# Performance work log

Measured on AMD Instinct MI355X. Metric: run time of the kernel, lower is better.

Reference implementation:

```python
import jax, jax.numpy as jnp
import numpy as np

L = 4        # n_layers_time
D = 128      # d_model
H = 8        # n_heads
T = 12       # n_time_bins (= max_n_time_bins)
E = 128      # n_electrodes
B = 2        # batch
S = 2        # n_samples (1 positive + 1 negative)
OUT = 1      # dim_output
ROPE_SCALE = 10000.0
HD = D // H          # head_dim = 16
HD4 = HD // 4        # rotated half-pair width = 4
EPS = 1e-5


def _rope_tables():
    # theta = scale ** ((-arange(0, hd//2, 2) / hd) // 2)  -- faithful to torch precedence
    a = jnp.arange(0, HD // 2, 2, dtype=jnp.float32)
    theta = ROPE_SCALE ** jnp.floor((-a / HD) / 2.0)       # [HD4]
    pe = jnp.arange(T, dtype=jnp.float32)[:, None] * theta  # [T, HD4]
    pe = pe.reshape(1, 1, T, 1, 1, HD4)
    return jnp.sin(pe), jnp.cos(pe)


def _causal_mask():
    return jnp.triu(jnp.ones((T, T), dtype=bool), k=1)  # True = masked


def layer_norm(x, g, b):
    m = jnp.mean(x, axis=-1, keepdims=True)
    v = jnp.mean(jnp.square(x - m), axis=-1, keepdims=True)
    return (x - m) * jax.lax.rsqrt(v + EPS) * g + b


def apply_rope(x, sin, cos):
    # x: [B, S, T, E, H, HD]
    xl = x[..., :HD4]
    xr = x[..., HD4:2 * HD4]
    xu = x[..., 2 * HD4:]
    return jnp.concatenate([xl * cos + xr * sin, xr * cos - xl * sin, xu], axis=-1)


def attention(q_in, k_in, v_in, Wq, bq, Wk, bk, Wv, bv, Wo, bo, sin, cos, causal):
    Bq, Sq, Tq, Eq, Dm = q_in.shape
    Sk = k_in.shape[1]
    proj = lambda x, W, b, Ss: (x @ W.T + b).reshape(Bq, Ss, Tq, Eq, H, HD)
    q = apply_rope(proj(q_in, Wq, bq, Sq), sin, cos)
    k = apply_rope(proj(k_in, Wk, bk, Sk), sin, cos)
    v = proj(v_in, Wv, bv, Sk)
    # flatten (S,T,E) -> seq
    qf = q.transpose(0, 4, 1, 2, 3, 5).reshape(Bq, H, Sq * Tq * Eq, HD)
    kf = k.transpose(0, 4, 1, 2, 3, 5).reshape(Bq, H, Sk * Tq * Eq, HD)
    vf = v.transpose(0, 4, 1, 2, 3, 5).reshape(Bq, H, Sk * Tq * Eq, HD)
    scores = jnp.einsum('bhqd,bhkd->bhqk', qf, kf) * (float(HD) ** -0.5)
    scores = scores.reshape(Bq, H, Sq, Tq, Eq, Sk, Tq, Eq)
    mask = causal[None, None, None, :, None, None, :, None]  # causal over time only
    scores = jnp.where(mask, -jnp.inf, scores)
    scores = scores.reshape(Bq, H, Sq * Tq * Eq, Sk * Tq * Eq)
    attnw = jax.nn.softmax(scores, axis=-1)
    attnw = jnp.where(jnp.isnan(attnw), 0.0, attnw)
    out = jnp.einsum('bhqk,bhkd->bhqd', attnw, vf)
    out = out.reshape(Bq, H, Sq, Tq, Eq, HD).transpose(0, 2, 3, 4, 1, 5).reshape(Bq, Sq, Tq, Eq, Dm)
    return out @ Wo.T + bo


def setup_inputs() -> dict:
    key = jax.random.key(0)
    ks = jax.random.split(key, 16)
    w = lambda k, shape: jax.random.normal(k, shape, dtype=jnp.float32) * 0.02
    inp = {
        'x': jax.random.normal(ks[0], (B, S, T, E, D), dtype=jnp.float32),
        'Wq': w(ks[1], (L, D, D)), 'bq': jnp.zeros((L, D), jnp.float32),
        'Wk': w(ks[2], (L, D, D)), 'bk': jnp.zeros((L, D), jnp.float32),
        'Wv': w(ks[3], (L, D, D)), 'bv': jnp.zeros((L, D), jnp.float32),
        'Wo': w(ks[4], (L, D, D)), 'bo': jnp.zeros((L, D), jnp.float32),
        'W1': w(ks[5], (L, 4 * D, D)), 'b1': jnp.zeros((L, 4 * D), jnp.float32),
        'W2': w(ks[6], (L, D, 4 * D)), 'b2': jnp.zeros((L, D), jnp.float32),
        'g1': jnp.ones((L, D), jnp.float32), 'bn1': jnp.zeros((L, D), jnp.float32),
        'g2': jnp.ones((L, D), jnp.float32), 'bn2': jnp.zeros((L, D), jnp.float32),
        'Wf': w(ks[7], (OUT, D)), 'bf': jnp.zeros((OUT,), jnp.float32),
    }
    return inp


def reference(x, Wq, bq, Wk, bk, Wv, bv, Wo, bo, W1, b1, W2, b2, g1, bn1, g2, bn2, Wf, bf):
    sin, cos = _rope_tables()
    causal = _causal_mask()
    for i in range(L):
        x2 = layer_norm(x, g1[i], bn1[i])
        kv = x2[:, :1]
        x_pos = attention(x2[:, :1], kv, kv, Wq[i], bq[i], Wk[i], bk[i], Wv[i], bv[i], Wo[i], bo[i], sin, cos, causal)
        x_neg = attention(x2[:, 1:], kv, kv, Wq[i], bq[i], Wk[i], bk[i], Wv[i], bv[i], Wo[i], bo[i], sin, cos, causal)
        x = jnp.concatenate([x[:, :1] + x_pos, x[:, 1:] + x_neg], axis=1)
        x2 = layer_norm(x, g2[i], bn2[i])
        h = jax.nn.gelu(x2 @ W1[i].T + b1[i], approximate=False)
        x = x + h @ W2[i].T + b2[i]
    return x @ Wf.T + bf
```

## Files before the change

### kernel.cpp

```cpp
#include <hip/hip_runtime.h>
#include <hip/hip_bf16.h>
#include <math.h>

#define LAYERS 4
#define DIM    128
#define NH     8
#define TT     12
#define EE     128
#define BB     2
#define SS     2
#define HD     16
#define DFF    512
#define NROWS  (BB*SS*TT*EE)
#define NKROWS (BB*TT*EE)

typedef __attribute__((ext_vector_type(8)))  short bf16x8;
typedef __attribute__((ext_vector_type(4)))  short short4v;
typedef __attribute__((ext_vector_type(4)))  float f32x4;
typedef __attribute__((ext_vector_type(16))) float f32x16;

#define MFMA32 __builtin_amdgcn_mfma_f32_32x32x16_bf16

__device__ __forceinline__ unsigned short f2bf(float f) {
    union { float f; unsigned u; } x; x.f = f;
    unsigned r = x.u + 0x7fffu + ((x.u >> 16) & 1u);
    return (unsigned short)(r >> 16);
}

__device__ __forceinline__ unsigned cvtpk(float a, float b) {
    unsigned r;
    asm("v_cvt_pk_bf16_f32 %0, %1, %2" : "=v"(r) : "v"(a), "v"(b));
    return r;
}

union U8 { unsigned u[4]; bf16x8 v; };

__global__ __launch_bounds__(256) void wconv_kernel(const float* __restrict__ Wq,
        const float* __restrict__ Wk, const float* __restrict__ Wv,
        const float* __restrict__ Wo, const float* __restrict__ W1,
        const float* __restrict__ W2, short* __restrict__ wbuf) {
    int idx = (blockIdx.x * 256 + threadIdx.x) * 4;
    const float* src; int off;
    if      (idx < 65536)  { src = Wq; off = idx; }
    else if (idx < 131072) { src = Wk; off = idx - 65536; }
    else if (idx < 196608) { src = Wv; off = idx - 131072; }
    else if (idx < 262144) { src = Wo; off = idx - 196608; }
    else if (idx < 524288) { src = W1; off = idx - 262144; }
    else                   { src = W2; off = idx - 524288; }
    float4 v = *(const float4*)(src + off);
    short4v o = { (short)f2bf(v.x), (short)f2bf(v.y), (short)f2bf(v.z), (short)f2bf(v.w) };
    *(short4v*)(wbuf + idx) = o;
}

__global__ __launch_bounds__(256) void ln_kernel(const float* __restrict__ x,
                                                 short* __restrict__ y,
                                                 const float* __restrict__ g,
                                                 const float* __restrict__ b) {
    int wave = threadIdx.x >> 6, lane = threadIdx.x & 63;
    int row = blockIdx.x * 4 + wave;
    const float* xp = x + (size_t)row * DIM;
    float2 v = *(const float2*)(xp + lane * 2);
    float s = v.x + v.y, sq = v.x * v.x + v.y * v.y;
    #pragma unroll
    for (int o = 1; o < 64; o <<= 1) { s += __shfl_xor(s, o); sq += __shfl_xor(sq, o); }
    float mean = s * (1.0f / 128.0f);
    float var = sq * (1.0f / 128.0f) - mean * mean;
    float rs = 1.0f / sqrtf(var + 1e-5f);
    float2 gv = *(const float2*)(g + lane * 2);
    float2 bv = *(const float2*)(b + lane * 2);
    float ox = (v.x - mean) * rs * gv.x + bv.x;
    float oy = (v.y - mean) * rs * gv.y + bv.y;
    unsigned u = (unsigned)f2bf(ox) | ((unsigned)f2bf(oy) << 16);
    *(unsigned*)(&y[(size_t)row * 128 + lane * 2]) = u;
}

__device__ __forceinline__ void gemm_core32(const short* __restrict__ Ab,
                                            const short* __restrict__ Wb,
                                            int K, f32x16 acc[2]) {
    #pragma unroll 8
    for (int k0 = 0; k0 < K; k0 += 16) {
        bf16x8 a0 = *(const bf16x8*)(Ab + k0);
        bf16x8 a1 = *(const bf16x8*)(Ab + (size_t)32 * K + k0);
        bf16x8 b  = *(const bf16x8*)(Wb + k0);
        acc[0] = MFMA32(a0, b, acc[0], 0, 0, 0);
        acc[1] = MFMA32(a1, b, acc[1], 0, 0, 0);
    }
}

__global__ __launch_bounds__(256) void qkv_kernel(const short* __restrict__ x2b,
        const short* __restrict__ wbuf, const float* __restrict__ bq,
        const float* __restrict__ bk, const float* __restrict__ bv, int layer,
        short* __restrict__ qb, short* __restrict__ kb, short* __restrict__ vt) {
    int z = blockIdx.z, by = blockIdx.y, bx = blockIdx.x;
    if (z > 0 && by >= 24) return;
    const short* Wz = wbuf + (z == 0 ? 0 : z == 1 ? 65536 : 131072) + layer * 16384;
    const float* bz = (z == 0 ? bq : z == 1 ? bk : bv) + layer * 128;
    int r0 = by * 128, c0 = bx * 64;
    int gadd = (z > 0) ? (by / 12) * 1536 : 0;
    int tid = threadIdx.x, wv = tid >> 6, l = tid & 63, l31 = l & 31, hi = l >> 5;
    int wr = wv >> 1, wc = wv & 1;
    const short* Ab = x2b + (size_t)(r0 + gadd + wr * 64 + l31) * 128 + hi * 8;
    const short* Wb = Wz + (size_t)(c0 + wc * 32 + l31) * 128 + hi * 8;
    f32x16 acc[2];
    #pragma unroll
    for (int i = 0; i < 16; ++i) { acc[0][i] = 0.f; acc[1][i] = 0.f; }
    gemm_core32(Ab, Wb, 128, acc);
    int c = c0 + wc * 32 + l31;
    float bb = bz[c];
    int t = by % 12;
    if (z < 2) {
        short* dst = z ? kb : qb;
        float sc = z ? 1.0f : 0.25f;
        int cc = c & 15, i4 = c & 3;
        float theta = (i4 == 0) ? 1.0f : 1e-4f;
        float ang = (float)t * theta;
        float sn = sinf(ang), cs = cosf(ang);
        #pragma unroll
        for (int mi = 0; mi < 2; ++mi)
        #pragma unroll
        for (int reg = 0; reg < 16; ++reg) {
            float v = acc[mi][reg] + bb;
            float pv = __shfl_xor(v, 4);
            float vo = (cc < 4) ? (v * cs + pv * sn)
                     : (cc < 8) ? (v * cs - pv * sn) : v;
            vo *= sc;
            int r = r0 + wr * 64 + mi * 32 + (reg & 3) + 8 * (reg >> 2) + 4 * hi;
            dst[(size_t)r * 128 + c] = (short)f2bf(vo);
        }
    } else {
        int d = c & 15, hh = c >> 4, bidx = by / 12;
        #pragma unroll
        for (int mi = 0; mi < 2; ++mi)
        #pragma unroll
        for (int rq = 0; rq < 4; ++rq) {
            int rcb = r0 + wr * 64 + mi * 32 + 8 * rq + 4 * hi;
            int kk = rcb - bidx * 1536;
            short4v o;
            #pragma unroll
            for (int j = 0; j < 4; ++j) o[j] = (short)f2bf(acc[mi][4 * rq + j] + bb);
            *(short4v*)(vt + ((size_t)(bidx * 8 + hh) * 16 + d) * 1536 + kk) = o;
        }
    }
}

__global__ __launch_bounds__(256) void attn_part(const short* __restrict__ qb,
        const short* __restrict__ kb, const short* __restrict__ vt,
        float* __restrict__ part) {
    int bid = blockIdx.x;
    int blk = bid / 3, sp = bid - blk * 3;
    int tq = 11 - (blk >> 5);
    int hb = blk & 31, h = hb >> 2, bs = hb & 3, b = bs >> 1;
    int tid = threadIdx.x;
    int wv = tid >> 6, l = tid & 63, l31 = l & 31, hi = l >> 5;
    int q0 = (bs * 12 + tq) * 128 + wv * 32;
    bf16x8 qf = *(const bf16x8*)(qb + (size_t)(q0 + l31) * 128 + h * 16 + hi * 8);
    const short* kp = kb + (size_t)(b * 1536 + l31) * 128 + h * 16 + hi * 8;
    const short* vp = vt + ((size_t)(b * 8 + h) * 16 + l31) * 1536 + hi * 8;
    bool vload = l31 < 16;
    f32x16 acc, zv;
    #pragma unroll
    for (int i = 0; i < 16; ++i) { acc[i] = 0.f; zv[i] = 0.f; }
    float m = -1e30f, lsum = 0.f;
    int nch = (tq + 1) * 4;
    for (int c = sp; c < nch; c += 3) {
        bf16x8 kf = *(const bf16x8*)(kp + (size_t)c * 32 * 128);
        f32x16 s = MFMA32(kf, qf, zv, 0, 0, 0);
        float cm = s[0];
        #pragma unroll
        for (int j = 1; j < 16; ++j) cm = fmaxf(cm, s[j]);
        cm = fmaxf(cm, __shfl_xor(cm, 32));
        float mn = fmaxf(m, cm);
        float corr = __expf(m - mn);
        m = mn;
        float p[16]; float ps = 0.f;
        #pragma unroll
        for (int j = 0; j < 16; ++j) { p[j] = __expf(s[j] - mn); ps += p[j]; }
        ps += __shfl_xor(ps, 32);
        lsum = lsum * corr + ps;
        #pragma unroll
        for (int r = 0; r < 8; ++r) acc[r] *= corr;
        unsigned w0 = cvtpk(p[0],  p[1]),  w1 = cvtpk(p[2],  p[3]);
        unsigned w2 = cvtpk(p[4],  p[5]),  w3 = cvtpk(p[6],  p[7]);
        unsigned w4 = cvtpk(p[8],  p[9]),  w5 = cvtpk(p[10], p[11]);
        unsigned w6 = cvtpk(p[12], p[13]), w7 = cvtpk(p[14], p[15]);
        unsigned t1 = hi ? w0 : w2, t2 = hi ? w1 : w3;
        unsigned t3 = hi ? w4 : w6, t4 = hi ? w5 : w7;
        unsigned x1 = __shfl_xor((int)t1, 32), x2 = __shfl_xor((int)t2, 32);
        unsigned x3 = __shfl_xor((int)t3, 32), x4 = __shfl_xor((int)t4, 32);
        U8 pb1, pb2;
        pb1.u[0] = hi ? x1 : w0;  pb1.u[1] = hi ? x2 : w1;
        pb1.u[2] = hi ? w2 : x1;  pb1.u[3] = hi ? w3 : x2;
        pb2.u[0] = hi ? x3 : w4;  pb2.u[1] = hi ? x4 : w5;
        pb2.u[2] = hi ? w6 : x3;  pb2.u[3] = hi ? w7 : x4;
        bf16x8 vf1, vf2;
        #pragma unroll
        for (int i = 0; i < 8; ++i) { vf1[i] = 0; vf2[i] = 0; }
        if (vload) {
            vf1 = *(const bf16x8*)(vp + c * 32);
            vf2 = *(const bf16x8*)(vp + c * 32 + 16);
        }
        acc = MFMA32(vf1, pb1.v, acc, 0, 0, 0);
        acc = MFMA32(vf2, pb2.v, acc, 0, 0, 0);
    }
    float* pp = part + ((size_t)bid * 256 + tid) * 10;
    pp[0] = m; pp[1] = lsum;
    #pragma unroll
    for (int j = 0; j < 8; ++j) pp[2 + j] = acc[j];
}

__global__ __launch_bounds__(256) void attn_comb(const float* __restrict__ part,
        short* __restrict__ attb) {
    int blk = blockIdx.x;
    int tq = 11 - (blk >> 5);
    int hb = blk & 31, h = hb >> 2, bs = hb & 3;
    int tid = threadIdx.x;
    int wv = tid >> 6, l = tid & 63, l31 = l & 31, hi = l >> 5;
    int q0 = (bs * 12 + tq) * 128 + wv * 32;
    const float* p0 = part + ((size_t)(blk * 3) * 256 + tid) * 10;
    const float* p1 = p0 + 2560;
    const float* p2 = p1 + 2560;
    float m0 = p0[0], m1 = p1[0], m2 = p2[0];
    float mm = fmaxf(fmaxf(m0, m1), m2);
    float e0 = __expf(m0 - mm), e1 = __expf(m1 - mm), e2 = __expf(m2 - mm);
    float lsum = p0[1] * e0 + p1[1] * e1 + p2[1] * e2;
    float linv = 1.0f / lsum;
    short4v o1, o2;
    #pragma unroll
    for (int j = 0; j < 4; ++j)
        o1[j] = (short)f2bf((p0[2 + j] * e0 + p1[2 + j] * e1 + p2[2 + j] * e2) * linv);
    #pragma unroll
    for (int j = 0; j < 4; ++j)
        o2[j] = (short)f2bf((p0[6 + j] * e0 + p1[6 + j] * e1 + p2[6 + j] * e2) * linv);
    size_t base = (size_t)(q0 + l31) * 128 + h * 16;
    *(short4v*)(attb + base + 4 * hi) = o1;
    *(short4v*)(attb + base + 8 + 4 * hi) = o2;
}

__global__ __launch_bounds__(256) void res_gemm(const short* __restrict__ A,
        const short* __restrict__ W, const float* __restrict__ bias,
        float* __restrict__ C, int K) {
    int by = blockIdx.y, bx = blockIdx.x;
    int r0 = by * 128, c0 = bx * 64;
    int tid = threadIdx.x, wv = tid >> 6, l = tid & 63, l31 = l & 31, hi = l >> 5;
    int wr = wv >> 1, wc = wv & 1;
    const short* Ab = A + (size_t)(r0 + wr * 64 + l31) * K + hi * 8;
    const short* Wb = W + (size_t)(c0 + wc * 32 + l31) * K + hi * 8;
    f32x16 acc[2];
    #pragma unroll
    for (int i = 0; i < 16; ++i) { acc[0][i] = 0.f; acc[1][i] = 0.f; }
    gemm_core32(Ab, Wb, K, acc);
    int c = c0 + wc * 32 + l31;
    float bb = bias[c];
    #pragma unroll
    for (int mi = 0; mi < 2; ++mi)
    #pragma unroll
    for (int reg = 0; reg < 16; ++reg) {
        int r = r0 + wr * 64 + mi * 32 + (reg & 3) + 8 * (reg >> 2) + 4 * hi;
        C[(size_t)r * 128 + c] += acc[mi][reg] + bb;
    }
}

__global__ __launch_bounds__(256) void gelu_gemm(const short* __restrict__ A,
        const short* __restrict__ W, const float* __restrict__ bias,
        short* __restrict__ H) {
    int by = blockIdx.y, bx = blockIdx.x;
    int r0 = by * 128, c0 = bx * 64;
    int tid = threadIdx.x, wv = tid >> 6, l = tid & 63, l31 = l & 31, hi = l >> 5;
    int wr = wv >> 1, wc = wv & 1;
    const short* Ab = A + (size_t)(r0 + wr * 64 + l31) * 128 + hi * 8;
    const short* Wb = W + (size_t)(c0 + wc * 32 + l31) * 128 + hi * 8;
    f32x16 acc[2];
    #pragma unroll
    for (int i = 0; i < 16; ++i) { acc[0][i] = 0.f; acc[1][i] = 0.f; }
    gemm_core32(Ab, Wb, 128, acc);
    int c = c0 + wc * 32 + l31;
    float bb = bias[c];
    #pragma unroll
    for (int mi = 0; mi < 2; ++mi)
    #pragma unroll
    for (int reg = 0; reg < 16; ++reg) {
        int r = r0 + wr * 64 + mi * 32 + (reg & 3) + 8 * (reg >> 2) + 4 * hi;
        float v = acc[mi][reg] + bb;
        v = 0.5f * v * (1.0f + erff(v * 0.70710678118654752f));
        H[(size_t)r * 512 + c] = (short)f2bf(v);
    }
}

__global__ __launch_bounds__(256) void final_kernel(const float* __restrict__ x,
        const float* __restrict__ Wf, const float* __restrict__ bf,
        float* __restrict__ out) {
    int wave = threadIdx.x >> 6, lane = threadIdx.x & 63;
    int row = blockIdx.x * 4 + wave;
    float2 xv = *(const float2*)(x + (size_t)row * DIM + lane * 2);
    float2 wv = *(const float2*)(Wf + lane * 2);
    float s = xv.x * wv.x + xv.y * wv.y;
    #pragma unroll
    for (int o = 1; o < 64; o <<= 1) s += __shfl_xor(s, o);
    if (lane == 0) out[row] = s + bf[0];
}

extern "C" void kernel_launch(void* const* d_in, const int* in_sizes, int n_in,
                              void* d_out, int out_size, void* d_ws, size_t ws_size,
                              hipStream_t stream) {
    const float* x   = (const float*)d_in[0];
    const float* Wq  = (const float*)d_in[1];
    const float* bq  = (const float*)d_in[2];
    const float* Wk  = (const float*)d_in[3];
    const float* bk  = (const float*)d_in[4];
    const float* Wv  = (const float*)d_in[5];
    const float* bv  = (const float*)d_in[6];
    const float* Wo  = (const float*)d_in[7];
    const float* bo  = (const float*)d_in[8];
    const float* W1  = (const float*)d_in[9];
    const float* b1  = (const float*)d_in[10];
    const float* W2  = (const float*)d_in[11];
    const float* b2  = (const float*)d_in[12];
    const float* g1  = (const float*)d_in[13];
    const float* bn1 = (const float*)d_in[14];
    const float* g2  = (const float*)d_in[15];
    const float* bn2 = (const float*)d_in[16];
    const float* Wf  = (const float*)d_in[17];
    const float* bf  = (const float*)d_in[18];
    float* out = (float*)d_out;

    char* wsb = (char*)d_ws;
    float* xcur  = (float*)(wsb + 0);
    short* x2b   = (short*)(wsb + 3145728);
    short* qb    = (short*)(wsb + 4718592);
    short* kb    = (short*)(wsb + 6291456);
    short* vt    = (short*)(wsb + 7077888);
    short* attb  = (short*)(wsb + 7864320);
    short* hb    = (short*)(wsb + 9437184);
    short* wbuf  = (short*)(wsb + 15728640);
    float* partb = (float*)(wsb + 17301504);

    hipMemcpyAsync(xcur, x, (size_t)NROWS * DIM * sizeof(float),
                   hipMemcpyDeviceToDevice, stream);
    wconv_kernel<<<768, 256, 0, stream>>>(Wq, Wk, Wv, Wo, W1, W2, wbuf);

    for (int i = 0; i < LAYERS; ++i) {
        const short* wob = wbuf + 196608 + i * 16384;
        const short* w1b = wbuf + 262144 + i * 65536;
        const short* w2b = wbuf + 524288 + i * 65536;

        ln_kernel<<<NROWS / 4, 256, 0, stream>>>(xcur, x2b, g1 + i * DIM, bn1 + i * DIM);
        qkv_kernel<<<dim3(2, 48, 3), 256, 0, stream>>>(x2b, wbuf, bq, bk, bv, i, qb, kb, vt);
        attn_part<<<1152, 256, 0, stream>>>(qb, kb, vt, partb);
        attn_comb<<<384, 256, 0, stream>>>(partb, attb);
        res_gemm<<<dim3(2, 48), 256, 0, stream>>>(attb, wob, bo + i * DIM, xcur, 128);
        ln_kernel<<<NROWS / 4, 256, 0, stream>>>(xcur, x2b, g2 + i * DIM, bn2 + i * DIM);
        gelu_gemm<<<dim3(8, 48), 256, 0, stream>>>(x2b, w1b, b1 + i * DFF, hb);
        res_gemm<<<dim3(2, 48), 256, 0, stream>>>(hb, w2b, b2 + i * DIM, xcur, 512);
    }
    final_kernel<<<NROWS / 4, 256, 0, stream>>>(xcur, Wf, bf, out);
}
```

Baseline: 369.2 us.

## Fuse LayerNorm into QKV and FFN1 GEMMs via LDS staging

Removes the standalone LayerNorm kernels. The QKV and FFN1 GEMMs now normalize their 128-row input tile straight into shared memory as bf16, using 512-thread blocks that cover a full 128-column output tile. The initial device-to-device copy of x is dropped: layer 0 reads the input directly, and res_gemm writes res+acc out-of-place. This cuts two launches per layer and the x2 bf16 round trip through global memory. In exchange, FFN1 recomputes LayerNorm four times per row tile, and QKV uses fewer, larger blocks.

Measured after the change: 366.7 us. About the same (-0.7%).

```diff
diff --git a/kernel.cpp b/kernel.cpp
--- a/kernel.cpp
+++ b/kernel.cpp
@@ -16,10 +16,10 @@
 
 typedef __attribute__((ext_vector_type(8)))  short bf16x8;
 typedef __attribute__((ext_vector_type(4)))  short short4v;
-typedef __attribute__((ext_vector_type(4)))  float f32x4;
 typedef __attribute__((ext_vector_type(16))) float f32x16;
 
 #define MFMA32 __builtin_amdgcn_mfma_f32_32x32x16_bf16
+#define CROW(reg) (((reg) & 3) + 8 * ((reg) >> 2) + 4 * hi)
 
 __device__ __forceinline__ unsigned short f2bf(float f) {
     union { float f; unsigned u; } x; x.f = f;
@@ -52,60 +52,74 @@
     *(short4v*)(wbuf + idx) = o;
 }
 
-__global__ __launch_bounds__(256) void ln_kernel(const float* __restrict__ x,
-                                                 short* __restrict__ y,
-                                                 const float* __restrict__ g,
-                                                 const float* __restrict__ b) {
-    int wave = threadIdx.x >> 6, lane = threadIdx.x & 63;
-    int row = blockIdx.x * 4 + wave;
-    const float* xp = x + (size_t)row * DIM;
-    float2 v = *(const float2*)(xp + lane * 2);
-    float s = v.x + v.y, sq = v.x * v.x + v.y * v.y;
-    #pragma unroll
-    for (int o = 1; o < 64; o <<= 1) { s += __shfl_xor(s, o); sq += __shfl_xor(sq, o); }
+__device__ __forceinline__ void ln_to_lds(short (*At)[136], const float* __restrict__ xrow0,
+                                          const float* __restrict__ gl,
+                                          const float* __restrict__ bl, int tid) {
+    int row = tid >> 2, sub = tid & 3;
+    const float* xp = xrow0 + (size_t)row * 128 + sub * 32;
+    float4 v[8];
+    float s = 0.f, q = 0.f;
+    #pragma unroll
+    for (int i = 0; i < 8; ++i) {
+        v[i] = *(const float4*)(xp + i * 4);
+        s += v[i].x + v[i].y + v[i].z + v[i].w;
+        q += v[i].x * v[i].x + v[i].y * v[i].y + v[i].z * v[i].z + v[i].w * v[i].w;
+    }
+    s += __shfl_xor(s, 1); q += __shfl_xor(q, 1);
+    s += __shfl_xor(s, 2); q += __shfl_xor(q, 2);
     float mean = s * (1.0f / 128.0f);
-    float var = sq * (1.0f / 128.0f) - mean * mean;
-    float rs = 1.0f / sqrtf(var + 1e-5f);
-    float2 gv = *(const float2*)(g + lane * 2);
-    float2 bv = *(const float2*)(b + lane * 2);
-    float ox = (v.x - mean) * rs * gv.x + bv.x;
-    float oy = (v.y - mean) * rs * gv.y + bv.y;
-    unsigned u = (unsigned)f2bf(ox) | ((unsigned)f2bf(oy) << 16);
-    *(unsigned*)(&y[(size_t)row * 128 + lane * 2]) = u;
-}
-
-__device__ __forceinline__ void gemm_core32(const short* __restrict__ Ab,
-                                            const short* __restrict__ Wb,
-                                            int K, f32x16 acc[2]) {
+    float rs = 1.0f / sqrtf(q * (1.0f / 128.0f) - mean * mean + 1e-5f);
+    const float* gp = gl + sub * 32;
+    const float* bp = bl + sub * 32;
+    #pragma unroll
+    for (int i = 0; i < 8; ++i) {
+        float4 g4 = *(const float4*)(gp + i * 4);
+        float4 b4 = *(const float4*)(bp + i * 4);
+        unsigned u0 = cvtpk((v[i].x - mean) * rs * g4.x + b4.x,
+                            (v[i].y - mean) * rs * g4.y + b4.y);
+        unsigned u1 = cvtpk((v[i].z - mean) * rs * g4.z + b4.z,
+                            (v[i].w - mean) * rs * g4.w + b4.w);
+        unsigned long long uu = (unsigned long long)u0 | ((unsigned long long)u1 << 32);
+        *(unsigned long long*)(&At[row][sub * 32 + i * 4]) = uu;
+    }
+}
+
+__global__ __launch_bounds__(512) void qkv_lds(const float* __restrict__ xin,
+        const short* __restrict__ wbuf, const float* __restrict__ bq,
+        const float* __restrict__ bk, const float* __restrict__ bv, int layer,
+        const float* __restrict__ gl, const float* __restrict__ bl,
+        short* __restrict__ qb, short* __restrict__ kb, short* __restrict__ vt) {
+    __shared__ short At[128][136];
+    int bid = blockIdx.x;
+    int z, by;
+    if (bid < 48)      { z = 0; by = bid; }
+    else if (bid < 72) { z = 1; by = bid - 48; }
+    else               { z = 2; by = bid - 72; }
+    const short* Wz = wbuf + (z == 0 ? 0 : z == 1 ? 65536 : 131072) + layer * 16384;
+    const float* bz = (z == 0 ? bq : z == 1 ? bk : bv) + layer * 128;
+    int r0 = by * 128;
+    int gadd = (z > 0) ? (by / 12) * 1536 : 0;
+    int tid = threadIdx.x;
+
+    ln_to_lds(At, xin + (size_t)(r0 + gadd) * 128, gl, bl, tid);
+    __syncthreads();
+
+    int wv = tid >> 6, l = tid & 63, l31 = l & 31, hi = l >> 5;
+    int wr = wv >> 2, wc = wv & 3;
+    const short* Wb = Wz + (size_t)(wc * 32 + l31) * 128 + hi * 8;
+    f32x16 acc[2];
+    #pragma unroll
+    for (int i = 0; i < 16; ++i) { acc[0][i] = 0.f; acc[1][i] = 0.f; }
     #pragma unroll 8
-    for (int k0 = 0; k0 < K; k0 += 16) {
-        bf16x8 a0 = *(const bf16x8*)(Ab + k0);
-        bf16x8 a1 = *(const bf16x8*)(Ab + (size_t)32 * K + k0);
+    for (int k0 = 0; k0 < 128; k0 += 16) {
+        bf16x8 a0 = *(const bf16x8*)(&At[wr * 64 + l31][k0 + hi * 8]);
+        bf16x8 a1 = *(const bf16x8*)(&At[wr * 64 + 32 + l31][k0 + hi * 8]);
         bf16x8 b  = *(const bf16x8*)(Wb + k0);
         acc[0] = MFMA32(a0, b, acc[0], 0, 0, 0);
         acc[1] = MFMA32(a1, b, acc[1], 0, 0, 0);
     }
-}
-
-__global__ __launch_bounds__(256) void qkv_kernel(const short* __restrict__ x2b,
-        const short* __restrict__ wbuf, const float* __restrict__ bq,
-        const float* __restrict__ bk, const float* __restrict__ bv, int layer,
-        short* __restrict__ qb, short* __restrict__ kb, short* __restrict__ vt) {
-    int z = blockIdx.z, by = blockIdx.y, bx = blockIdx.x;
-    if (z > 0 && by >= 24) return;
-    const short* Wz = wbuf + (z == 0 ? 0 : z == 1 ? 65536 : 131072) + layer * 16384;
-    const float* bz = (z == 0 ? bq : z == 1 ? bk : bv) + layer * 128;
-    int r0 = by * 128, c0 = bx * 64;
-    int gadd = (z > 0) ? (by / 12) * 1536 : 0;
-    int tid = threadIdx.x, wv = tid >> 6, l = tid & 63, l31 = l & 31, hi = l >> 5;
-    int wr = wv >> 1, wc = wv & 1;
-    const short* Ab = x2b + (size_t)(r0 + gadd + wr * 64 + l31) * 128 + hi * 8;
-    const short* Wb = Wz + (size_t)(c0 + wc * 32 + l31) * 128 + hi * 8;
-    f32x16 acc[2];
-    #pragma unroll
-    for (int i = 0; i < 16; ++i) { acc[0][i] = 0.f; acc[1][i] = 0.f; }
-    gemm_core32(Ab, Wb, 128, acc);
-    int c = c0 + wc * 32 + l31;
+
+    int c = wc * 32 + l31;
     float bb = bz[c];
     int t = by % 12;
     if (z < 2) {
@@ -124,7 +138,7 @@
             float vo = (cc < 4) ? (v * cs + pv * sn)
                      : (cc < 8) ? (v * cs - pv * sn) : v;
             vo *= sc;
-            int r = r0 + wr * 64 + mi * 32 + (reg & 3) + 8 * (reg >> 2) + 4 * hi;
+            int r = r0 + wr * 64 + mi * 32 + CROW(reg);
             dst[(size_t)r * 128 + c] = (short)f2bf(vo);
         }
     } else {
@@ -236,9 +250,22 @@
     *(short4v*)(attb + base + 8 + 4 * hi) = o2;
 }
 
+__device__ __forceinline__ void gemm_core32(const short* __restrict__ Ab,
+                                            const short* __restrict__ Wb,
+                                            int K, f32x16 acc[2]) {
+    #pragma unroll 8
+    for (int k0 = 0; k0 < K; k0 += 16) {
+        bf16x8 a0 = *(const bf16x8*)(Ab + k0);
+        bf16x8 a1 = *(const bf16x8*)(Ab + (size_t)32 * K + k0);
+        bf16x8 b  = *(const bf16x8*)(Wb + k0);
+        acc[0] = MFMA32(a0, b, acc[0], 0, 0, 0);
+        acc[1] = MFMA32(a1, b, acc[1], 0, 0, 0);
+    }
+}
+
 __global__ __launch_bounds__(256) void res_gemm(const short* __restrict__ A,
         const short* __restrict__ W, const float* __restrict__ bias,
-        float* __restrict__ C, int K) {
+        const float* __restrict__ res, float* __restrict__ C, int K) {
     int by = blockIdx.y, bx = blockIdx.x;
     int r0 = by * 128, c0 = bx * 64;
     int tid = threadIdx.x, wv = tid >> 6, l = tid & 63, l31 = l & 31, hi = l >> 5;
@@ -255,31 +282,45 @@
     for (int mi = 0; mi < 2; ++mi)
     #pragma unroll
     for (int reg = 0; reg < 16; ++reg) {
-        int r = r0 + wr * 64 + mi * 32 + (reg & 3) + 8 * (reg >> 2) + 4 * hi;
-        C[(size_t)r * 128 + c] += acc[mi][reg] + bb;
-    }
-}
-
-__global__ __launch_bounds__(256) void gelu_gemm(const short* __restrict__ A,
-        const short* __restrict__ W, const float* __restrict__ bias,
+        int r = r0 + wr * 64 + mi * 32 + CROW(reg);
+        size_t ix = (size_t)r * 128 + c;
+        C[ix] = res[ix] + acc[mi][reg] + bb;
+    }
+}
+
+__global__ __launch_bounds__(512) void ffn1_lds(const float* __restrict__ xin,
+        const short* __restrict__ w1l, const float* __restrict__ b1l,
+        const float* __restrict__ gl, const float* __restrict__ bl,
         short* __restrict__ H) {
+    __shared__ short At[128][136];
     int by = blockIdx.y, bx = blockIdx.x;
-    int r0 = by * 128, c0 = bx * 64;
-    int tid = threadIdx.x, wv = tid >> 6, l = tid & 63, l31 = l & 31, hi = l >> 5;
-    int wr = wv >> 1, wc = wv & 1;
-    const short* Ab = A + (size_t)(r0 + wr * 64 + l31) * 128 + hi * 8;
-    const short* Wb = W + (size_t)(c0 + wc * 32 + l31) * 128 + hi * 8;
+    int r0 = by * 128;
+    int tid = threadIdx.x;
+
+    ln_to_lds(At, xin + (size_t)r0 * 128, gl, bl, tid);
+    __syncthreads();
+
+    int wv = tid >> 6, l = tid & 63, l31 = l & 31, hi = l >> 5;
+    int wr = wv >> 2, wc = wv & 3;
+    int c = bx * 128 + wc * 32 + l31;
+    const short* Wb = w1l + (size_t)c * 128 + hi * 8;
     f32x16 acc[2];
     #pragma unroll
     for (int i = 0; i < 16; ++i) { acc[0][i] = 0.f; acc[1][i] = 0.f; }
-    gemm_core32(Ab, Wb, 128, acc);
-    int c = c0 + wc * 32 + l31;
-    float bb = bias[c];
+    #pragma unroll 8
+    for (int k0 = 0; k0 < 128; k0 += 16) {
+        bf16x8 a0 = *(const bf16x8*)(&At[wr * 64 + l31][k0 + hi * 8]);
+        bf16x8 a1 = *(const bf16x8*)(&At[wr * 64 + 32 + l31][k0 + hi * 8]);
+        bf16x8 b  = *(const bf16x8*)(Wb + k0);
+        acc[0] = MFMA32(a0, b, acc[0], 0, 0, 0);
+        acc[1] = MFMA32(a1, b, acc[1], 0, 0, 0);
+    }
+    float bb = b1l[c];
     #pragma unroll
     for (int mi = 0; mi < 2; ++mi)
     #pragma unroll
     for (int reg = 0; reg < 16; ++reg) {
-        int r = r0 + wr * 64 + mi * 32 + (reg & 3) + 8 * (reg >> 2) + 4 * hi;
+        int r = r0 + wr * 64 + mi * 32 + CROW(reg);
         float v = acc[mi][reg] + bb;
         v = 0.5f * v * (1.0f + erff(v * 0.70710678118654752f));
         H[(size_t)r * 512 + c] = (short)f2bf(v);
@@ -325,7 +366,6 @@
 
     char* wsb = (char*)d_ws;
     float* xcur  = (float*)(wsb + 0);
-    short* x2b   = (short*)(wsb + 3145728);
     short* qb    = (short*)(wsb + 4718592);
     short* kb    = (short*)(wsb + 6291456);
     short* vt    = (short*)(wsb + 7077888);
@@ -334,23 +374,24 @@
     short* wbuf  = (short*)(wsb + 15728640);
     float* partb = (float*)(wsb + 17301504);
 
-    hipMemcpyAsync(xcur, x, (size_t)NROWS * DIM * sizeof(float),
-                   hipMemcpyDeviceToDevice, stream);
     wconv_kernel<<<768, 256, 0, stream>>>(Wq, Wk, Wv, Wo, W1, W2, wbuf);
 
     for (int i = 0; i < LAYERS; ++i) {
         const short* wob = wbuf + 196608 + i * 16384;
         const short* w1b = wbuf + 262144 + i * 65536;
         const short* w2b = wbuf + 524288 + i * 65536;
-
-        ln_kernel<<<NROWS / 4, 256, 0, stream>>>(xcur, x2b, g1 + i * DIM, bn1 + i * DIM);
-        qkv_kernel<<<dim3(2, 48, 3), 256, 0, stream>>>(x2b, wbuf, bq, bk, bv, i, qb, kb, vt);
+        const float* xin = (i == 0) ? x : xcur;
+
+        qkv_lds<<<96, 512, 0, stream>>>(xin, wbuf, bq, bk, bv, i,
+                g1 + i * DIM, bn1 + i * DIM, qb, kb, vt);
         attn_part<<<1152, 256, 0, stream>>>(qb, kb, vt, partb);
         attn_comb<<<384, 256, 0, stream>>>(partb, attb);
-        res_gemm<<<dim3(2, 48), 256, 0, stream>>>(attb, wob, bo + i * DIM, xcur, 128);
-        ln_kernel<<<NROWS / 4, 256, 0, stream>>>(xcur, x2b, g2 + i * DIM, bn2 + i * DIM);
-        gelu_gemm<<<dim3(8, 48), 256, 0, stream>>>(x2b, w1b, b1 + i * DFF, hb);
-        res_gemm<<<dim3(2, 48), 256, 0, stream>>>(hb, w2b, b2 + i * DIM, xcur, 512);
+        res_gemm<<<dim3(2, 48), 256, 0, stream>>>(attb, wob, bo + i * DIM,
+                xin, xcur, 128);
+        ffn1_lds<<<dim3(4, 48), 512, 0, stream>>>(xcur, w1b, b1 + i * DFF,
+                g2 + i * DIM, bn2 + i * DIM, hb);
+        res_gemm<<<dim3(2, 48), 256, 0, stream>>>(hb, w2b, b2 + i * DIM,
+                xcur, xcur, 512);
     }
     final_kernel<<<NROWS / 4, 256, 0, stream>>>(xcur, Wf, bf, out);
 }
```
